# Kernel tuning notes

Measured on AMD Instinct MI355X. Metric: run time of the kernel, lower is better.

The kernel has to match this reference:

```python
import jax, jax.numpy as jnp
import numpy as np

EPS = 1e-5

def layer_norm(x, g, b):
    m = jnp.mean(x, axis=-1, keepdims=True)
    v = jnp.var(x, axis=-1, keepdims=True)
    return (x - m) / jnp.sqrt(v + EPS) * g + b


def setup_inputs() -> dict:
    key = jax.random.key(0)
    ks = jax.random.split(key, 12)
    B, L, D = 4, 4096, 512
    DF = 2 * D  # dim * dim_ff_scale
    inp = {
        "x": jax.random.normal(ks[0], (B, L, D), dtype=jnp.float32),
        "hidden_real": jax.random.normal(ks[1], (B, D), dtype=jnp.float32),
        "hidden_imag": jax.random.normal(ks[2], (B, D), dtype=jnp.float32),
        # SpiralConv complex params (real/imag parts), as torch.randn cfloat
        "phazor_re": jax.random.normal(ks[3], (D,), dtype=jnp.float32),
        "phazor_im": jax.random.normal(ks[4], (D,), dtype=jnp.float32),
        "pinit_re": jax.random.normal(ks[5], (D,), dtype=jnp.float32),
        "pinit_im": jax.random.normal(ks[6], (D,), dtype=jnp.float32),
        # shared LayerNorm params
        "ln_g": jnp.ones((D,), dtype=jnp.float32),
        "ln_b": jnp.zeros((D,), dtype=jnp.float32),
        # FFN params
        "w1": jax.random.normal(ks[7], (D, DF), dtype=jnp.float32) * (1.0 / np.sqrt(D)),
        "b1": jnp.zeros((DF,), dtype=jnp.float32),
        "w2": jax.random.normal(ks[8], (DF, D), dtype=jnp.float32) * (1.0 / np.sqrt(DF)),
        "b2": jnp.zeros((D,), dtype=jnp.float32),
    }
    return inp


def reference(x, hidden_real, hidden_imag, phazor_re, phazor_im,
              pinit_re, pinit_im, ln_g, ln_b, w1, b1, w2, b2):
    B, L, D = x.shape
    p = jax.lax.complex(phazor_re, phazor_im)
    pinit = jax.lax.complex(pinit_re, pinit_im)
    hidden_last = jax.lax.complex(hidden_real, hidden_imag)

    # phazor = p/|p| * exp(-|p|)  (unit direction, decaying magnitude)
    absp = jnp.abs(p)
    phazor = p / absp * jnp.exp(-absp)

    # phazor_progression[t, d] = phazor[d] ** t
    t = jnp.arange(L, dtype=jnp.float32)
    prog = jnp.exp(t[:, None] * jnp.log(phazor)[None, :])  # [L, D] complex
    filt = prog * pinit[None, :]                            # [L, D]

    x_res = x
    xn = layer_norm(x, ln_g, ln_b)

    # FFT long convolution along sequence, zero-padded to 2L (linear conv)
    filt_fft = jnp.fft.fft(filt, n=2 * L, axis=0)           # [2L, D]
    x_fft = jnp.fft.fft(xn, n=2 * L, axis=1)                # [B, 2L, D]
    conv = jnp.fft.ifft(filt_fft[None, :, :] * x_fft, axis=1)[:, :L, :]

    hidden = conv + hidden_last[:, None, :] * prog[None, :, :] * phazor[None, None, :]

    y = hidden.real + x_res
    yn = layer_norm(y, ln_g, ln_b)
    h = yn @ w1 + b1
    h = h * jax.nn.sigmoid(h)  # SiLU; dropout=0 (eval) is identity
    out = h @ w2 + b2 + y
    return out, hidden
```

## Files before the change

kernel.cpp:

```cpp
#include <hip/hip_runtime.h>
#include <hip/hip_bf16.h>
#include <math.h>

#define BB 4
#define LL 4096
#define DD 512
#define DF 1024
#define CHUNKS 64
#define LC 64
#define HALF_ROWS 8192

typedef __bf16 bf16x8 __attribute__((ext_vector_type(8)));
typedef float f32x4 __attribute__((ext_vector_type(4)));

__device__ inline void get_phazor(const float* __restrict__ pre, const float* __restrict__ pim,
                                  int d, float& ar, float& ai) {
    float pr = pre[d], pi = pim[d];
    float ab = sqrtf(pr * pr + pi * pi);
    float sc = expf(-ab) / ab;
    ar = pr * sc;
    ai = pi * sc;
}

__global__ __launch_bounds__(256) void k_wt(const float* __restrict__ w1, const float* __restrict__ w2,
                                            __bf16* __restrict__ w1t, __bf16* __restrict__ w2t) {
    __shared__ float tile[32][33];
    const float* src;
    __bf16* dst;
    int R, C;
    if (blockIdx.y == 0) { src = w1; dst = w1t; R = DD; C = DF; }
    else                 { src = w2; dst = w2t; R = DF; C = DD; }
    int ntx = C / 32;
    int c0 = (blockIdx.x % ntx) * 32, r0 = (blockIdx.x / ntx) * 32;
    int tx = threadIdx.x & 31, ty = threadIdx.x >> 5;
#pragma unroll
    for (int i = 0; i < 32; i += 8)
        tile[ty + i][tx] = src[(size_t)(r0 + ty + i) * C + c0 + tx];
    __syncthreads();
#pragma unroll
    for (int i = 0; i < 32; i += 8)
        dst[(size_t)(c0 + ty + i) * R + r0 + tx] = (__bf16)tile[tx][ty + i];
}

__global__ __launch_bounds__(256) void k_xstats(const float* __restrict__ x, float* __restrict__ xstats) {
    int wave = threadIdx.x >> 6, lane = threadIdx.x & 63;
    size_t row = (size_t)blockIdx.x * 4 + wave;
    const float4* xr = reinterpret_cast<const float4*>(x + row * DD) + lane * 2;
    float4 a = xr[0], b = xr[1];
    float s = a.x + a.y + a.z + a.w + b.x + b.y + b.z + b.w;
    float q = a.x * a.x + a.y * a.y + a.z * a.z + a.w * a.w +
              b.x * b.x + b.y * b.y + b.z * b.z + b.w * b.w;
#pragma unroll
    for (int off = 32; off; off >>= 1) {
        s += __shfl_down(s, off);
        q += __shfl_down(q, off);
    }
    if (lane == 0) {
        float m = s * (1.0f / DD);
        float v = q * (1.0f / DD) - m * m;
        xstats[row * 2 + 0] = m;
        xstats[row * 2 + 1] = rsqrtf(v + 1e-5f);
    }
}

__global__ __launch_bounds__(512) void k_scan_partial(
    const float* __restrict__ x, const float* __restrict__ xstats,
    const float* __restrict__ pre, const float* __restrict__ pim,
    const float* __restrict__ pinr, const float* __restrict__ pini,
    const float* __restrict__ g, const float* __restrict__ bvec,
    float* __restrict__ carry) {
    int d = threadIdx.x;
    int c = blockIdx.x % CHUNKS, b = blockIdx.x / CHUNKS;
    float ar, ai;
    get_phazor(pre, pim, d, ar, ai);
    float pr = pinr[d], pi = pini[d];
    float gd = g[d], bd = bvec[d];
    float hr = 0.f, hi = 0.f;
    int l0 = c * LC;
    const float* xp = x + ((size_t)b * LL + l0) * DD + d;
    const float* st = xstats + ((size_t)b * LL + l0) * 2;
    for (int i = 0; i < LC; i++) {
        float m = st[2 * i], r = st[2 * i + 1];
        float xn = (xp[(size_t)i * DD] - m) * r * gd + bd;
        float ur = pr * xn, ui = pi * xn;
        float t = ar * hr - ai * hi + ur;
        hi = ar * hi + ai * hr + ui;
        hr = t;
    }
    size_t idx = ((size_t)blockIdx.x * DD + d) * 2;
    carry[idx] = hr;
    carry[idx + 1] = hi;
}

__global__ __launch_bounds__(512) void k_chunk_scan(
    const float* __restrict__ hr0, const float* __restrict__ hi0,
    const float* __restrict__ pre, const float* __restrict__ pim,
    const float* __restrict__ carry, float* __restrict__ carry_in) {
    int d = threadIdx.x, b = blockIdx.x;
    float ar, ai;
    get_phazor(pre, pim, d, ar, ai);
    float sr = ar, si = ai;
#pragma unroll
    for (int i = 0; i < 6; i++) {
        float t = sr * sr - si * si;
        si = 2.f * sr * si;
        sr = t;
    }
    float cr = hr0[b * DD + d], ci = hi0[b * DD + d];
    for (int k = 0; k < CHUNKS; k++) {
        size_t idx = (((size_t)b * CHUNKS + k) * DD + d) * 2;
        carry_in[idx] = cr;
        carry_in[idx + 1] = ci;
        float tr = carry[idx], ti = carry[idx + 1];
        float t = sr * cr - si * ci + tr;
        ci = sr * ci + si * cr + ti;
        cr = t;
    }
}

template <int MODE>
__global__ __launch_bounds__(512) void k_scan_out(
    const float* __restrict__ x, const float* __restrict__ xstats,
    const float* __restrict__ pre, const float* __restrict__ pim,
    const float* __restrict__ pinr, const float* __restrict__ pini,
    const float* __restrict__ g, const float* __restrict__ bvec,
    const float* __restrict__ carry_in,
    float* __restrict__ out_y, float* __restrict__ hid) {
    int d = threadIdx.x;
    int c = blockIdx.x % CHUNKS, b = blockIdx.x / CHUNKS;
    float ar, ai;
    get_phazor(pre, pim, d, ar, ai);
    float pr = pinr[d], pi = pini[d];
    float gd = g[d], bd = bvec[d];
    size_t cidx = ((size_t)blockIdx.x * DD + d) * 2;
    float hr = carry_in[cidx], hi = carry_in[cidx + 1];
    int l0 = c * LC;
    const float* xp = x + ((size_t)b * LL + l0) * DD + d;
    const float* st = xstats + ((size_t)b * LL + l0) * 2;
    for (int i = 0; i < LC; i++) {
        float m = st[2 * i], r = st[2 * i + 1];
        float xv = xp[(size_t)i * DD];
        float xn = (xv - m) * r * gd + bd;
        float ur = pr * xn, ui = pi * xn;
        float t = ar * hr - ai * hi + ur;
        hi = ar * hi + ai * hr + ui;
        hr = t;
        size_t row = (size_t)b * LL + l0 + i;
        if constexpr (MODE == 0) {
            out_y[row * DD + d] = hr + xv;
        } else if constexpr (MODE == 1) {
            hid[row * DD + d] = hr;
        } else if constexpr (MODE == 2) {
            reinterpret_cast<float2*>(hid)[row * DD + d] = make_float2(hr, hi);
        } else {
            out_y[row * DD + d] = hr + xv;
            hid[row * DD + d] = hr;
        }
    }
}

__global__ __launch_bounds__(256) void k_ynorm(const float* __restrict__ y,
                                               const float* __restrict__ g, const float* __restrict__ bvec,
                                               __bf16* __restrict__ yn) {
    int wave = threadIdx.x >> 6, lane = threadIdx.x & 63;
    size_t row = (size_t)blockIdx.x * 4 + wave;
    const float4* yr = reinterpret_cast<const float4*>(y + row * DD) + lane * 2;
    float4 a = yr[0], b = yr[1];
    float s = a.x + a.y + a.z + a.w + b.x + b.y + b.z + b.w;
    float q = a.x * a.x + a.y * a.y + a.z * a.z + a.w * a.w +
              b.x * b.x + b.y * b.y + b.z * b.z + b.w * b.w;
#pragma unroll
    for (int off = 32; off; off >>= 1) {
        s += __shfl_xor(s, off);
        q += __shfl_xor(q, off);
    }
    float m = s * (1.0f / DD);
    float r = rsqrtf(q * (1.0f / DD) - m * m + 1e-5f);
    int dbase = lane * 8;
    const float4* gp = reinterpret_cast<const float4*>(g + dbase);
    const float4* bp = reinterpret_cast<const float4*>(bvec + dbase);
    float4 g0 = gp[0], g1 = gp[1], b0 = bp[0], b1 = bp[1];
    bf16x8 o;
    o[0] = (__bf16)((a.x - m) * r * g0.x + b0.x);
    o[1] = (__bf16)((a.y - m) * r * g0.y + b0.y);
    o[2] = (__bf16)((a.z - m) * r * g0.z + b0.z);
    o[3] = (__bf16)((a.w - m) * r * g0.w + b0.w);
    o[4] = (__bf16)((b.x - m) * r * g1.x + b1.x);
    o[5] = (__bf16)((b.y - m) * r * g1.y + b1.y);
    o[6] = (__bf16)((b.z - m) * r * g1.z + b1.z);
    o[7] = (__bf16)((b.w - m) * r * g1.w + b1.w);
    *reinterpret_cast<bf16x8*>(yn + row * DD + dbase) = o;
}

template <int KDIM, int NDIM, int EPI>
__global__ __launch_bounds__(256) void k_gemm(
    const __bf16* __restrict__ A, const __bf16* __restrict__ Bt,
    const float* __restrict__ bias, const float* __restrict__ yadd,
    float* __restrict__ outf, __bf16* __restrict__ outb) {
    __shared__ __align__(16) __bf16 As[128 * 64];
    __shared__ __align__(16) __bf16 Bs[128 * 64];
    constexpr int NT = NDIM / 128;
    int nwg = gridDim.x;
    int bid = blockIdx.x;
    int swz = (bid & 7) * (nwg >> 3) + (bid >> 3);
    int m0 = (swz / NT) * 128;
    int n0 = (swz % NT) * 128;
    int tid = threadIdx.x;
    int wave = tid >> 6, lane = tid & 63;

    f32x4 acc[4][4] = {};

    int wm = (wave & 1) * 64, wn = (wave >> 1) * 64;
    int fr = lane & 15;
    int qbase = lane >> 4;

    for (int k0 = 0; k0 < KDIM; k0 += 64) {
        __syncthreads();
#pragma unroll
        for (int i = 0; i < 4; i++) {
            int c = tid + i * 256;
            int row = c >> 3, kq = c & 7;
            int kqg = kq ^ (row & 7);
            const __bf16* ga = A + (size_t)(m0 + row) * KDIM + k0 + kqg * 8;
            const __bf16* gb = Bt + (size_t)(n0 + row) * KDIM + k0 + kqg * 8;
            __bf16* la = As + (size_t)(i * 256 + wave * 64) * 8;
            __bf16* lb = Bs + (size_t)(i * 256 + wave * 64) * 8;
            __builtin_amdgcn_global_load_lds((const __attribute__((address_space(1))) unsigned int*)ga,
                                             (__attribute__((address_space(3))) unsigned int*)la, 16, 0, 0);
            __builtin_amdgcn_global_load_lds((const __attribute__((address_space(1))) unsigned int*)gb,
                                             (__attribute__((address_space(3))) unsigned int*)lb, 16, 0, 0);
        }
        __syncthreads();
#pragma unroll
        for (int ks = 0; ks < 2; ks++) {
            int q = ks * 4 + qbase;
            bf16x8 af[4], bfv[4];
#pragma unroll
            for (int mi = 0; mi < 4; mi++) {
                int R = wm + mi * 16 + fr;
                af[mi] = *reinterpret_cast<const bf16x8*>(As + R * 64 + ((q ^ (R & 7)) << 3));
            }
#pragma unroll
            for (int ni = 0; ni < 4; ni++) {
                int R = wn + ni * 16 + fr;
                bfv[ni] = *reinterpret_cast<const bf16x8*>(Bs + R * 64 + ((q ^ (R & 7)) << 3));
            }
#pragma unroll
            for (int mi = 0; mi < 4; mi++)
#pragma unroll
                for (int ni = 0; ni < 4; ni++)
                    acc[mi][ni] = __builtin_amdgcn_mfma_f32_16x16x32_bf16(af[mi], bfv[ni], acc[mi][ni], 0, 0, 0);
        }
    }

    int orow = (lane >> 4) * 4;
    int ocol = lane & 15;
#pragma unroll
    for (int mi = 0; mi < 4; mi++) {
#pragma unroll
        for (int ni = 0; ni < 4; ni++) {
            int gr = m0 + wm + mi * 16 + orow;
            int gc = n0 + wn + ni * 16 + ocol;
            float bv = bias[gc];
#pragma unroll
            for (int j = 0; j < 4; j++) {
                float v = acc[mi][ni][j] + bv;
                size_t idx = (size_t)(gr + j) * NDIM + gc;
                if constexpr (EPI == 1) {
                    float sv = v / (1.0f + __expf(-v));
                    outb[idx] = (__bf16)sv;
                } else {
                    outf[idx] = v + yadd[idx];
                }
            }
        }
    }
}

extern "C" void kernel_launch(void* const* d_in, const int* in_sizes, int n_in,
                              void* d_out, int out_size, void* d_ws, size_t ws_size,
                              hipStream_t stream) {
    const float* x = (const float*)d_in[0];
    const float* hr0 = (const float*)d_in[1];
    const float* hi0 = (const float*)d_in[2];
    const float* pre = (const float*)d_in[3];
    const float* pim = (const float*)d_in[4];
    const float* pinr = (const float*)d_in[5];
    const float* pini = (const float*)d_in[6];
    const float* lng = (const float*)d_in[7];
    const float* lnb = (const float*)d_in[8];
    const float* w1 = (const float*)d_in[9];
    const float* b1 = (const float*)d_in[10];
    const float* w2 = (const float*)d_in[11];
    const float* b2 = (const float*)d_in[12];

    const size_t n = (size_t)BB * LL * DD;
    float* outp = (float*)d_out;
    char* hidbase = (char*)d_out + n * 4;
    float* hidp = (float*)hidbase;
    bool interleaved = (out_size >= (int)(3 * n));

    char* ws = (char*)d_ws;
    float* xstats = (float*)ws;      ws += (size_t)BB * LL * 2 * 4;
    float* carry = (float*)ws;       ws += (size_t)BB * CHUNKS * DD * 8;
    float* carry_in = (float*)ws;    ws += (size_t)BB * CHUNKS * DD * 8;
    __bf16* w1t = (__bf16*)ws;       ws += (size_t)DD * DF * 2;
    __bf16* w2t = (__bf16*)ws;       ws += (size_t)DF * DD * 2;
    char* ws_big = ws;
    const size_t SMALL = (size_t)(128 + 1024 + 1024 + 1024 + 1024) * 1024;
    const size_t NEED_FULL = SMALL + ((size_t)48 << 20);
    const size_t NEED_HALF = SMALL + ((size_t)24 << 20);

    k_wt<<<dim3((DD / 32) * (DF / 32), 2), 256, 0, stream>>>(w1, w2, w1t, w2t);
    k_xstats<<<(BB * LL) / 4, 256, 0, stream>>>(x, xstats);
    k_scan_partial<<<BB * CHUNKS, 512, 0, stream>>>(x, xstats, pre, pim, pinr, pini, lng, lnb, carry);
    k_chunk_scan<<<BB, 512, 0, stream>>>(hr0, hi0, pre, pim, carry, carry_in);

    if (!interleaved && ws_size >= NEED_FULL) {
        __bf16* yn = (__bf16*)ws_big;
        __bf16* h1 = (__bf16*)(ws_big + ((size_t)16 << 20));
        k_scan_out<3><<<BB * CHUNKS, 512, 0, stream>>>(x, xstats, pre, pim, pinr, pini, lng, lnb,
                                                       carry_in, outp, hidp);
        k_ynorm<<<(BB * LL) / 4, 256, 0, stream>>>(outp, lng, lnb, yn);
        k_gemm<DD, DF, 1><<<(BB * LL / 128) * (DF / 128), 256, 0, stream>>>(
            yn, w1t, b1, nullptr, nullptr, h1);
        k_gemm<DF, DD, 2><<<(BB * LL / 128) * (DD / 128), 256, 0, stream>>>(
            h1, w2t, b2, outp, outp, nullptr);
    } else if (!interleaved && ws_size >= NEED_HALF) {
        __bf16* yn_h = (__bf16*)ws_big;
        __bf16* h1_h = (__bf16*)(ws_big + ((size_t)8 << 20));
        k_scan_out<3><<<BB * CHUNKS, 512, 0, stream>>>(x, xstats, pre, pim, pinr, pini, lng, lnb,
                                                       carry_in, outp, hidp);
        for (int h = 0; h < 2; h++) {
            float* yh = outp + (size_t)h * HALF_ROWS * DD;
            k_ynorm<<<HALF_ROWS / 4, 256, 0, stream>>>(yh, lng, lnb, yn_h);
            k_gemm<DD, DF, 1><<<(HALF_ROWS / 128) * (DF / 128), 256, 0, stream>>>(
                yn_h, w1t, b1, nullptr, nullptr, h1_h);
            k_gemm<DF, DD, 2><<<(HALF_ROWS / 128) * (DD / 128), 256, 0, stream>>>(
                h1_h, w2t, b2, yh, yh, nullptr);
        }
    } else {
        __bf16* yn_h = (__bf16*)hidbase;
        __bf16* h1_h = (__bf16*)(hidbase + ((size_t)8 << 20));
        k_scan_out<0><<<BB * CHUNKS, 512, 0, stream>>>(x, xstats, pre, pim, pinr, pini, lng, lnb,
                                                       carry_in, outp, nullptr);
        for (int h = 0; h < 2; h++) {
            float* yh = outp + (size_t)h * HALF_ROWS * DD;
            k_ynorm<<<HALF_ROWS / 4, 256, 0, stream>>>(yh, lng, lnb, yn_h);
            k_gemm<DD, DF, 1><<<(HALF_ROWS / 128) * (DF / 128), 256, 0, stream>>>(
                yn_h, w1t, b1, nullptr, nullptr, h1_h);
            k_gemm<DF, DD, 2><<<(HALF_ROWS / 128) * (DD / 128), 256, 0, stream>>>(
                h1_h, w2t, b2, yh, yh, nullptr);
        }
        if (interleaved) {
            k_scan_out<2><<<BB * CHUNKS, 512, 0, stream>>>(x, xstats, pre, pim, pinr, pini, lng, lnb,
                                                           carry_in, nullptr, hidp);
        } else {
            k_scan_out<1><<<BB * CHUNKS, 512, 0, stream>>>(x, xstats, pre, pim, pinr, pini, lng, lnb,
                                                           carry_in, nullptr, hidp);
        }
    }
}
```

Baseline: 116.2 us.

## Double-buffer GEMM LDS tiles and enlarge tiles to 512-thread blocks

```diff
diff --git a/kernel.cpp b/kernel.cpp
--- a/kernel.cpp
+++ b/kernel.cpp
@@ -192,73 +192,94 @@
     *reinterpret_cast<bf16x8*>(yn + row * DD + dbase) = o;
 }
 
-template <int KDIM, int NDIM, int EPI>
-__global__ __launch_bounds__(256) void k_gemm(
+template <int BM, int BN, int KDIM, int NDIM, int EPI>
+__global__ __launch_bounds__(512) void k_gemm(
     const __bf16* __restrict__ A, const __bf16* __restrict__ Bt,
     const float* __restrict__ bias, const float* __restrict__ yadd,
     float* __restrict__ outf, __bf16* __restrict__ outb) {
-    __shared__ __align__(16) __bf16 As[128 * 64];
-    __shared__ __align__(16) __bf16 Bs[128 * 64];
-    constexpr int NT = NDIM / 128;
+    __shared__ __align__(16) __bf16 As[2][BM * 64];
+    __shared__ __align__(16) __bf16 Bs[2][BN * 64];
+    constexpr int NT = NDIM / BN;
+    constexpr int MR = BM / 32;
+    constexpr int NR = BN / 64;
     int nwg = gridDim.x;
     int bid = blockIdx.x;
     int swz = (bid & 7) * (nwg >> 3) + (bid >> 3);
-    int m0 = (swz / NT) * 128;
-    int n0 = (swz % NT) * 128;
+    int m0 = (swz / NT) * BM;
+    int n0 = (swz % NT) * BN;
     int tid = threadIdx.x;
-    int wave = tid >> 6, lane = tid & 63;
-
-    f32x4 acc[4][4] = {};
-
-    int wm = (wave & 1) * 64, wn = (wave >> 1) * 64;
+    int wid = tid >> 6, lane = tid & 63;
+
+    f32x4 acc[MR][NR] = {};
+
+    int wm = (wid >> 2) * (BM / 2), wn = (wid & 3) * (BN / 4);
     int fr = lane & 15;
     int qbase = lane >> 4;
 
-    for (int k0 = 0; k0 < KDIM; k0 += 64) {
-        __syncthreads();
-#pragma unroll
-        for (int i = 0; i < 4; i++) {
-            int c = tid + i * 256;
+    auto stage = [&](int buf, int k0) {
+#pragma unroll
+        for (int i = 0; i < BM / 64; i++) {
+            int c = tid + i * 512;
             int row = c >> 3, kq = c & 7;
             int kqg = kq ^ (row & 7);
             const __bf16* ga = A + (size_t)(m0 + row) * KDIM + k0 + kqg * 8;
-            const __bf16* gb = Bt + (size_t)(n0 + row) * KDIM + k0 + kqg * 8;
-            __bf16* la = As + (size_t)(i * 256 + wave * 64) * 8;
-            __bf16* lb = Bs + (size_t)(i * 256 + wave * 64) * 8;
+            __bf16* la = &As[buf][(size_t)(i * 512 + wid * 64) * 8];
             __builtin_amdgcn_global_load_lds((const __attribute__((address_space(1))) unsigned int*)ga,
                                              (__attribute__((address_space(3))) unsigned int*)la, 16, 0, 0);
+        }
+#pragma unroll
+        for (int i = 0; i < BN / 64; i++) {
+            int c = tid + i * 512;
+            int row = c >> 3, kq = c & 7;
+            int kqg = kq ^ (row & 7);
+            const __bf16* gb = Bt + (size_t)(n0 + row) * KDIM + k0 + kqg * 8;
+            __bf16* lb = &Bs[buf][(size_t)(i * 512 + wid * 64) * 8];
             __builtin_amdgcn_global_load_lds((const __attribute__((address_space(1))) unsigned int*)gb,
                                              (__attribute__((address_space(3))) unsigned int*)lb, 16, 0, 0);
         }
-        __syncthreads();
+    };
+
+    auto compute = [&](int buf) {
 #pragma unroll
         for (int ks = 0; ks < 2; ks++) {
             int q = ks * 4 + qbase;
-            bf16x8 af[4], bfv[4];
-#pragma unroll
-            for (int mi = 0; mi < 4; mi++) {
+            bf16x8 af[MR], bfv[NR];
+#pragma unroll
+            for (int mi = 0; mi < MR; mi++) {
                 int R = wm + mi * 16 + fr;
-                af[mi] = *reinterpret_cast<const bf16x8*>(As + R * 64 + ((q ^ (R & 7)) << 3));
+                af[mi] = *reinterpret_cast<const bf16x8*>(&As[buf][R * 64 + ((q ^ (R & 7)) << 3)]);
             }
 #pragma unroll
-            for (int ni = 0; ni < 4; ni++) {
+            for (int ni = 0; ni < NR; ni++) {
                 int R = wn + ni * 16 + fr;
-                bfv[ni] = *reinterpret_cast<const bf16x8*>(Bs + R * 64 + ((q ^ (R & 7)) << 3));
+                bfv[ni] = *reinterpret_cast<const bf16x8*>(&Bs[buf][R * 64 + ((q ^ (R & 7)) << 3)]);
             }
 #pragma unroll
-            for (int mi = 0; mi < 4; mi++)
-#pragma unroll
-                for (int ni = 0; ni < 4; ni++)
-                    acc[mi][ni] = __builtin_amdgcn_mfma_f32_16x16x32_bf16(af[mi], bfv[ni], acc[mi][ni], 0, 0, 0);
-        }
-    }
+            for (int mi = 0; mi < MR; mi++)
+#pragma unroll
+                for (int ni = 0; ni < NR; ni++)
+                    acc[mi][ni] = __builtin_amdgcn_mfma_f32_16x16x32_bf16(af[mi], bfv[ni],
+                                                                          acc[mi][ni], 0, 0, 0);
+        }
+    };
+
+    stage(0, 0);
+    __syncthreads();
+    int cur = 0;
+    for (int k0 = 64; k0 < KDIM; k0 += 64) {
+        stage(cur ^ 1, k0);
+        compute(cur);
+        __syncthreads();
+        cur ^= 1;
+    }
+    compute(cur);
 
     int orow = (lane >> 4) * 4;
     int ocol = lane & 15;
 #pragma unroll
-    for (int mi = 0; mi < 4; mi++) {
-#pragma unroll
-        for (int ni = 0; ni < 4; ni++) {
+    for (int mi = 0; mi < MR; mi++) {
+#pragma unroll
+        for (int ni = 0; ni < NR; ni++) {
             int gr = m0 + wm + mi * 16 + orow;
             int gc = n0 + wn + ni * 16 + ocol;
             float bv = bias[gc];
@@ -322,9 +343,9 @@
         k_scan_out<3><<<BB * CHUNKS, 512, 0, stream>>>(x, xstats, pre, pim, pinr, pini, lng, lnb,
                                                        carry_in, outp, hidp);
         k_ynorm<<<(BB * LL) / 4, 256, 0, stream>>>(outp, lng, lnb, yn);
-        k_gemm<DD, DF, 1><<<(BB * LL / 128) * (DF / 128), 256, 0, stream>>>(
+        k_gemm<256, 256, DD, DF, 1><<<(BB * LL / 256) * (DF / 256), 512, 0, stream>>>(
             yn, w1t, b1, nullptr, nullptr, h1);
-        k_gemm<DF, DD, 2><<<(BB * LL / 128) * (DD / 128), 256, 0, stream>>>(
+        k_gemm<128, 256, DF, DD, 2><<<(BB * LL / 128) * (DD / 256), 512, 0, stream>>>(
             h1, w2t, b2, outp, outp, nullptr);
     } else if (!interleaved && ws_size >= NEED_HALF) {
         __bf16* yn_h = (__bf16*)ws_big;
@@ -334,9 +355,9 @@
         for (int h = 0; h < 2; h++) {
             float* yh = outp + (size_t)h * HALF_ROWS * DD;
             k_ynorm<<<HALF_ROWS / 4, 256, 0, stream>>>(yh, lng, lnb, yn_h);
-            k_gemm<DD, DF, 1><<<(HALF_ROWS / 128) * (DF / 128), 256, 0, stream>>>(
+            k_gemm<256, 256, DD, DF, 1><<<(HALF_ROWS / 256) * (DF / 256), 512, 0, stream>>>(
                 yn_h, w1t, b1, nullptr, nullptr, h1_h);
-            k_gemm<DF, DD, 2><<<(HALF_ROWS / 128) * (DD / 128), 256, 0, stream>>>(
+            k_gemm<128, 256, DF, DD, 2><<<(HALF_ROWS / 128) * (DD / 256), 512, 0, stream>>>(
                 h1_h, w2t, b2, yh, yh, nullptr);
         }
     } else {
@@ -347,9 +368,9 @@
         for (int h = 0; h < 2; h++) {
             float* yh = outp + (size_t)h * HALF_ROWS * DD;
             k_ynorm<<<HALF_ROWS / 4, 256, 0, stream>>>(yh, lng, lnb, yn_h);
-            k_gemm<DD, DF, 1><<<(HALF_ROWS / 128) * (DF / 128), 256, 0, stream>>>(
+            k_gemm<256, 256, DD, DF, 1><<<(HALF_ROWS / 256) * (DF / 256), 512, 0, stream>>>(
                 yn_h, w1t, b1, nullptr, nullptr, h1_h);
-            k_gemm<DF, DD, 2><<<(HALF_ROWS / 128) * (DD / 128), 256, 0, stream>>>(
+            k_gemm<128, 256, DF, DD, 2><<<(HALF_ROWS / 128) * (DD / 256), 512, 0, stream>>>(
                 h1_h, w2t, b2, yh, yh, nullptr);
         }
         if (interleaved) {
```

New measurement: 115.6 us. Within noise of the previous version (-0.5%).
